# Kernel tuning notes

Hardware: AMD Instinct MI355X
Metric: run time of the kernel (lower is better)

## Reference

```python
import jax, jax.numpy as jnp
import numpy as np

NC = 100000   # output rows of the sparse matrix
NT = 100000   # input columns of the sparse matrix
NNZ = 640000  # number of nonzeros (COO entries)
D = 128       # dense feature width


def setup_inputs() -> dict:
    key = jax.random.key(0)
    k1, k2, k3 = jax.random.split(key, 3)
    mat = jax.random.normal(k1, (NT, D), dtype=jnp.float32)
    row = jax.random.randint(k2, (NNZ,), 0, NC, dtype=jnp.int32)
    col = jax.random.randint(k3, (NNZ,), 0, NT, dtype=jnp.int32)
    return {"mat": mat, "row": row, "col": col}


def reference(mat, row, col):
    # Sparse binary (Nc x Nt) @ dense (Nt x D):
    # out[r] += mat[c] for each nonzero (r, c).
    # The TF original batches gather + tensor_scatter_nd_add over the
    # index list; a single gather + segment_sum computes the same result.
    vals = jnp.take(mat, col, axis=0)                      # [nnz, D]
    out = jax.ops.segment_sum(vals, row, num_segments=NC)  # [Nc, D]
    return out
```

## Files before the change

### kernel.cpp

```cpp
#include <hip/hip_runtime.h>


#define NC_CONST 100000
#define NNZ_CONST 640000
#define D_CONST 128
#define OVF_MAX 65536
#define NXCD 8
#define RANGE 12500
#define PLACE_BLOCKS 2048
#define SCAN_BLK 256
#define NBLK ((NC_CONST + SCAN_BLK - 1) / SCAN_BLK)

typedef float v4f __attribute__((ext_vector_type(4)));
typedef unsigned short u16;
typedef u16 v4u16 __attribute__((ext_vector_type(4)));

template <int CAP>
__global__ __launch_bounds__(256) void place_xcd_kernel(
    const int* __restrict__ row, const int* __restrict__ col,
    int* __restrict__ cnt, int* __restrict__ ovf_cnt,
    int* __restrict__ ovf, int* __restrict__ bucket) {
    const int xcd = blockIdx.x % NXCD;
    const int gidx = blockIdx.x / NXCD;
    const int lo = xcd * RANGE;
    const int hi = lo + RANGE;
    const int nthreads = (PLACE_BLOCKS / NXCD) * 256;
    const int4* row4 = reinterpret_cast<const int4*>(row);
    const int4* col4 = reinterpret_cast<const int4*>(col);
    const int n4 = NNZ_CONST / 4;

    for (int i = gidx * 256 + threadIdx.x; i < n4; i += nthreads) {
        int4 r4 = row4[i];
        int4 c4 = col4[i];
        #pragma unroll
        for (int k = 0; k < 4; ++k) {
            int r = (&r4.x)[k];
            if (r >= lo && r < hi) {
                int c = (&c4.x)[k];
                int idx = atomicAdd(&cnt[r], 1);
                if (idx < CAP) {
                    bucket[(size_t)r * CAP + idx] = c;
                } else {
                    int o = atomicAdd(ovf_cnt, 1);
                    if (o < OVF_MAX) { ovf[2 * o] = r; ovf[2 * o + 1] = c; }
                }
            }
        }
    }
}

__global__ __launch_bounds__(256) void convert_bf16_kernel(
    const float* __restrict__ mat, u16* __restrict__ matb) {
    const long long total4 = (long long)NC_CONST * D_CONST / 4;
    long long i = (long long)blockIdx.x * blockDim.x + threadIdx.x;
    if (i >= total4) return;
    const float4 v = reinterpret_cast<const float4*>(mat)[i];
    v4u16 o;
    #pragma unroll
    for (int k = 0; k < 4; ++k) {
        unsigned u = __float_as_uint((&v.x)[k]);
        o[k] = (u16)((u + 0x7FFFu + ((u >> 16) & 1u)) >> 16);
    }
    reinterpret_cast<v4u16*>(matb)[i] = o;
}

template <int CAP>
__global__ __launch_bounds__(256) void segsum_bf16_kernel(
    const u16* __restrict__ matb, const int* __restrict__ cnt,
    const int* __restrict__ ovf_cnt, const int* __restrict__ ovf,
    const int* __restrict__ bucket, float* __restrict__ out) {
    const int xcd = blockIdx.x % NXCD;
    const int local = blockIdx.x / NXCD;
    int g = xcd * RANGE + local * 8 + (threadIdx.x >> 5);
    int lane = threadIdx.x & 31;
    if (g >= xcd * RANGE + RANGE) return;

    int n = cnt[g];
    if (n > CAP) n = CAP;

    int myc = (lane < n) ? bucket[(size_t)g * CAP + lane] : 0;

    float ax = 0.f, ay = 0.f, az = 0.f, aw = 0.f;
    for (int j = 0; j < n; ++j) {
        int c = __shfl(myc, j, 32);
        const v4u16 b = reinterpret_cast<const v4u16*>(
            matb + (size_t)c * D_CONST)[lane];
        ax += __uint_as_float((unsigned)b[0] << 16);
        ay += __uint_as_float((unsigned)b[1] << 16);
        az += __uint_as_float((unsigned)b[2] << 16);
        aw += __uint_as_float((unsigned)b[3] << 16);
    }

    int novf = *ovf_cnt;
    if (novf > OVF_MAX) novf = OVF_MAX;
    for (int o = 0; o < novf; ++o) {
        if (ovf[2 * o] == g) {
            int c = ovf[2 * o + 1];
            const v4u16 b = reinterpret_cast<const v4u16*>(
                matb + (size_t)c * D_CONST)[lane];
            ax += __uint_as_float((unsigned)b[0] << 16);
            ay += __uint_as_float((unsigned)b[1] << 16);
            az += __uint_as_float((unsigned)b[2] << 16);
            aw += __uint_as_float((unsigned)b[3] << 16);
        }
    }

    v4f r;
    r.x = ax; r.y = ay; r.z = az; r.w = aw;
    __builtin_nontemporal_store(
        r, reinterpret_cast<v4f*>(out + (size_t)g * D_CONST) + lane);
}

template <int CAP>
__global__ __launch_bounds__(256) void segsum_xcd_kernel(
    const float* __restrict__ mat, const int* __restrict__ cnt,
    const int* __restrict__ ovf_cnt, const int* __restrict__ ovf,
    const int* __restrict__ bucket, float* __restrict__ out) {
    const int xcd = blockIdx.x % NXCD;
    const int local = blockIdx.x / NXCD;
    int g = xcd * RANGE + local * 8 + (threadIdx.x >> 5);
    int lane = threadIdx.x & 31;
    if (g >= xcd * RANGE + RANGE) return;

    int n = cnt[g];
    if (n > CAP) n = CAP;
    int myc = (lane < n) ? bucket[(size_t)g * CAP + lane] : 0;

    float ax = 0.f, ay = 0.f, az = 0.f, aw = 0.f;
    for (int j = 0; j < n; ++j) {
        int c = __shfl(myc, j, 32);
        const float4 v =
            reinterpret_cast<const float4*>(mat + (size_t)c * D_CONST)[lane];
        ax += v.x; ay += v.y; az += v.z; aw += v.w;
    }
    int novf = *ovf_cnt;
    if (novf > OVF_MAX) novf = OVF_MAX;
    for (int o = 0; o < novf; ++o) {
        if (ovf[2 * o] == g) {
            int c = ovf[2 * o + 1];
            const float4 v =
                reinterpret_cast<const float4*>(mat + (size_t)c * D_CONST)[lane];
            ax += v.x; ay += v.y; az += v.z; aw += v.w;
        }
    }
    v4f r;
    r.x = ax; r.y = ay; r.z = az; r.w = aw;
    __builtin_nontemporal_store(
        r, reinterpret_cast<v4f*>(out + (size_t)g * D_CONST) + lane);
}

__global__ __launch_bounds__(256) void scatter_add_kernel(
    const float* __restrict__ mat, const int* __restrict__ row,
    const int* __restrict__ col, float* __restrict__ out) {
    int gid = blockIdx.x * blockDim.x + threadIdx.x;
    int nz = gid >> 5;
    int lane = gid & 31;
    if (nz >= NNZ_CONST) return;
    int r = row[nz];
    int c = col[nz];
    const float4 v =
        reinterpret_cast<const float4*>(mat + (size_t)c * D_CONST)[lane];
    float* o = out + (size_t)r * D_CONST + (size_t)lane * 4;
    atomicAdd(o + 0, v.x);
    atomicAdd(o + 1, v.y);
    atomicAdd(o + 2, v.z);
    atomicAdd(o + 3, v.w);
}

extern "C" void kernel_launch(void* const* d_in, const int* in_sizes, int n_in,
                              void* d_out, int out_size, void* d_ws, size_t ws_size,
                              hipStream_t stream) {
    const float* mat = (const float*)d_in[0];
    const int* row   = (const int*)d_in[1];
    const int* col   = (const int*)d_in[2];
    float* out = (float*)d_out;

    constexpr int CAP = 32;
    const size_t ints_common =
        (size_t)NC_CONST + 1 + 2 * OVF_MAX + (size_t)NC_CONST * CAP;
    const size_t need_bf16 =
        (size_t)NC_CONST * D_CONST * sizeof(u16) + ints_common * sizeof(int);
    const size_t need_fp32 = ints_common * sizeof(int);

    const int seg_blocks = ((RANGE + 7) / 8) * NXCD;

    if (ws_size >= need_bf16) {
        u16* matb    = (u16*)d_ws;
        int* cnt     = (int*)(matb + (size_t)NC_CONST * D_CONST);
        int* ovf_cnt = cnt + NC_CONST;
        int* ovf     = ovf_cnt + 1;
        int* bucket  = ovf + 2 * OVF_MAX;

        (void)hipMemsetAsync(cnt, 0, (size_t)(NC_CONST + 1) * sizeof(int), stream);

        place_xcd_kernel<CAP><<<PLACE_BLOCKS, 256, 0, stream>>>(
            row, col, cnt, ovf_cnt, ovf, bucket);

        const long long total4 = (long long)NC_CONST * D_CONST / 4;
        convert_bf16_kernel<<<(int)((total4 + 255) / 256), 256, 0, stream>>>(
            mat, matb);

        segsum_bf16_kernel<CAP><<<seg_blocks, 256, 0, stream>>>(
            matb, cnt, ovf_cnt, ovf, bucket, out);
    } else if (ws_size >= need_fp32) {
        int* cnt     = (int*)d_ws;
        int* ovf_cnt = cnt + NC_CONST;
        int* ovf     = ovf_cnt + 1;
        int* bucket  = ovf + 2 * OVF_MAX;

        (void)hipMemsetAsync(cnt, 0, (size_t)(NC_CONST + 1) * sizeof(int), stream);

        place_xcd_kernel<CAP><<<PLACE_BLOCKS, 256, 0, stream>>>(
            row, col, cnt, ovf_cnt, ovf, bucket);
        segsum_xcd_kernel<CAP><<<seg_blocks, 256, 0, stream>>>(
            mat, cnt, ovf_cnt, ovf, bucket, out);
    } else {
        (void)hipMemsetAsync(out, 0, (size_t)out_size * sizeof(float), stream);
        const long long total = (long long)NNZ_CONST * 32;
        scatter_add_kernel<<<(int)((total + 255) / 256), 256, 0, stream>>>(
            mat, row, col, out);
    }
}
```

Baseline: 175.7 us.

## Fuse bucket placement with bf16 conversion and unroll gather loop by four

Merges the COO bucket-placement kernel and the fp32-to-bf16 conversion into one grid-stride kernel, removing a launch and letting the atomic-bound placement overlap with the streaming conversion. The segment-sum gather loop is unrolled by four so several independent row loads are in flight per warp. Nontemporal loads are added for the mat read and the bucket indices, and the overflow scan is skipped when empty. The fused kernel's fixed grid of 2048 blocks may give the conversion less parallelism than its previous dedicated launch.

```diff
diff --git a/kernel.cpp b/kernel.cpp
--- a/kernel.cpp
+++ b/kernel.cpp
@@ -8,18 +8,22 @@
 #define NXCD 8
 #define RANGE 12500
 #define PLACE_BLOCKS 2048
-#define SCAN_BLK 256
-#define NBLK ((NC_CONST + SCAN_BLK - 1) / SCAN_BLK)
 
 typedef float v4f __attribute__((ext_vector_type(4)));
 typedef unsigned short u16;
 typedef u16 v4u16 __attribute__((ext_vector_type(4)));
 
-template <int CAP>
-__global__ __launch_bounds__(256) void place_xcd_kernel(
+__device__ __forceinline__ float bf16_to_f32(u16 b) {
+    return __uint_as_float((unsigned)b << 16);
+}
+
+template <int CAP>
+__global__ __launch_bounds__(256) void place_convert_kernel(
     const int* __restrict__ row, const int* __restrict__ col,
+    const float* __restrict__ mat,
     int* __restrict__ cnt, int* __restrict__ ovf_cnt,
-    int* __restrict__ ovf, int* __restrict__ bucket) {
+    int* __restrict__ ovf, int* __restrict__ bucket,
+    u16* __restrict__ matb) {
     const int xcd = blockIdx.x % NXCD;
     const int gidx = blockIdx.x / NXCD;
     const int lo = xcd * RANGE;
@@ -47,21 +51,21 @@
             }
         }
     }
-}
-
-__global__ __launch_bounds__(256) void convert_bf16_kernel(
-    const float* __restrict__ mat, u16* __restrict__ matb) {
+
     const long long total4 = (long long)NC_CONST * D_CONST / 4;
-    long long i = (long long)blockIdx.x * blockDim.x + threadIdx.x;
-    if (i >= total4) return;
-    const float4 v = reinterpret_cast<const float4*>(mat)[i];
-    v4u16 o;
-    #pragma unroll
-    for (int k = 0; k < 4; ++k) {
-        unsigned u = __float_as_uint((&v.x)[k]);
-        o[k] = (u16)((u + 0x7FFFu + ((u >> 16) & 1u)) >> 16);
-    }
-    reinterpret_cast<v4u16*>(matb)[i] = o;
+    const long long stride = (long long)gridDim.x * 256;
+    for (long long i = (long long)blockIdx.x * 256 + threadIdx.x;
+         i < total4; i += stride) {
+        const v4f v = __builtin_nontemporal_load(
+            reinterpret_cast<const v4f*>(mat) + i);
+        v4u16 o;
+        #pragma unroll
+        for (int k = 0; k < 4; ++k) {
+            unsigned u = __float_as_uint(v[k]);
+            o[k] = (u16)((u + 0x7FFFu + ((u >> 16) & 1u)) >> 16);
+        }
+        reinterpret_cast<v4u16*>(matb)[i] = o;
+    }
 }
 
 template <int CAP>
@@ -78,30 +82,46 @@
     int n = cnt[g];
     if (n > CAP) n = CAP;
 
-    int myc = (lane < n) ? bucket[(size_t)g * CAP + lane] : 0;
+    int myc = (lane < n)
+        ? __builtin_nontemporal_load(bucket + (size_t)g * CAP + lane) : 0;
 
     float ax = 0.f, ay = 0.f, az = 0.f, aw = 0.f;
-    for (int j = 0; j < n; ++j) {
+    int j = 0;
+    for (; j + 4 <= n; j += 4) {
+        int c0 = __shfl(myc, j + 0, 32);
+        int c1 = __shfl(myc, j + 1, 32);
+        int c2 = __shfl(myc, j + 2, 32);
+        int c3 = __shfl(myc, j + 3, 32);
+        const v4u16 b0 = reinterpret_cast<const v4u16*>(matb + (size_t)c0 * D_CONST)[lane];
+        const v4u16 b1 = reinterpret_cast<const v4u16*>(matb + (size_t)c1 * D_CONST)[lane];
+        const v4u16 b2 = reinterpret_cast<const v4u16*>(matb + (size_t)c2 * D_CONST)[lane];
+        const v4u16 b3 = reinterpret_cast<const v4u16*>(matb + (size_t)c3 * D_CONST)[lane];
+        ax += bf16_to_f32(b0[0]) + bf16_to_f32(b1[0]) + bf16_to_f32(b2[0]) + bf16_to_f32(b3[0]);
+        ay += bf16_to_f32(b0[1]) + bf16_to_f32(b1[1]) + bf16_to_f32(b2[1]) + bf16_to_f32(b3[1]);
+        az += bf16_to_f32(b0[2]) + bf16_to_f32(b1[2]) + bf16_to_f32(b2[2]) + bf16_to_f32(b3[2]);
+        aw += bf16_to_f32(b0[3]) + bf16_to_f32(b1[3]) + bf16_to_f32(b2[3]) + bf16_to_f32(b3[3]);
+    }
+    for (; j < n; ++j) {
         int c = __shfl(myc, j, 32);
-        const v4u16 b = reinterpret_cast<const v4u16*>(
-            matb + (size_t)c * D_CONST)[lane];
-        ax += __uint_as_float((unsigned)b[0] << 16);
-        ay += __uint_as_float((unsigned)b[1] << 16);
-        az += __uint_as_float((unsigned)b[2] << 16);
-        aw += __uint_as_float((unsigned)b[3] << 16);
+        const v4u16 b = reinterpret_cast<const v4u16*>(matb + (size_t)c * D_CONST)[lane];
+        ax += bf16_to_f32(b[0]);
+        ay += bf16_to_f32(b[1]);
+        az += bf16_to_f32(b[2]);
+        aw += bf16_to_f32(b[3]);
     }
 
     int novf = *ovf_cnt;
-    if (novf > OVF_MAX) novf = OVF_MAX;
-    for (int o = 0; o < novf; ++o) {
-        if (ovf[2 * o] == g) {
-            int c = ovf[2 * o + 1];
-            const v4u16 b = reinterpret_cast<const v4u16*>(
-                matb + (size_t)c * D_CONST)[lane];
-            ax += __uint_as_float((unsigned)b[0] << 16);
-            ay += __uint_as_float((unsigned)b[1] << 16);
-            az += __uint_as_float((unsigned)b[2] << 16);
-            aw += __uint_as_float((unsigned)b[3] << 16);
+    if (novf > 0) {
+        if (novf > OVF_MAX) novf = OVF_MAX;
+        for (int o = 0; o < novf; ++o) {
+            if (ovf[2 * o] == g) {
+                int c = ovf[2 * o + 1];
+                const v4u16 b = reinterpret_cast<const v4u16*>(matb + (size_t)c * D_CONST)[lane];
+                ax += bf16_to_f32(b[0]);
+                ay += bf16_to_f32(b[1]);
+                az += bf16_to_f32(b[2]);
+                aw += bf16_to_f32(b[3]);
+            }
         }
     }
 
@@ -147,6 +167,40 @@
     r.x = ax; r.y = ay; r.z = az; r.w = aw;
     __builtin_nontemporal_store(
         r, reinterpret_cast<v4f*>(out + (size_t)g * D_CONST) + lane);
+}
+
+template <int CAP>
+__global__ __launch_bounds__(256) void place_xcd_kernel(
+    const int* __restrict__ row, const int* __restrict__ col,
+    int* __restrict__ cnt, int* __restrict__ ovf_cnt,
+    int* __restrict__ ovf, int* __restrict__ bucket) {
+    const int xcd = blockIdx.x % NXCD;
+    const int gidx = blockIdx.x / NXCD;
+    const int lo = xcd * RANGE;
+    const int hi = lo + RANGE;
+    const int nthreads = (PLACE_BLOCKS / NXCD) * 256;
+    const int4* row4 = reinterpret_cast<const int4*>(row);
+    const int4* col4 = reinterpret_cast<const int4*>(col);
+    const int n4 = NNZ_CONST / 4;
+
+    for (int i = gidx * 256 + threadIdx.x; i < n4; i += nthreads) {
+        int4 r4 = row4[i];
+        int4 c4 = col4[i];
+        #pragma unroll
+        for (int k = 0; k < 4; ++k) {
+            int r = (&r4.x)[k];
+            if (r >= lo && r < hi) {
+                int c = (&c4.x)[k];
+                int idx = atomicAdd(&cnt[r], 1);
+                if (idx < CAP) {
+                    bucket[(size_t)r * CAP + idx] = c;
+                } else {
+                    int o = atomicAdd(ovf_cnt, 1);
+                    if (o < OVF_MAX) { ovf[2 * o] = r; ovf[2 * o + 1] = c; }
+                }
+            }
+        }
+    }
 }
 
 __global__ __launch_bounds__(256) void scatter_add_kernel(
@@ -193,12 +247,8 @@
 
         (void)hipMemsetAsync(cnt, 0, (size_t)(NC_CONST + 1) * sizeof(int), stream);
 
-        place_xcd_kernel<CAP><<<PLACE_BLOCKS, 256, 0, stream>>>(
-            row, col, cnt, ovf_cnt, ovf, bucket);
-
-        const long long total4 = (long long)NC_CONST * D_CONST / 4;
-        convert_bf16_kernel<<<(int)((total4 + 255) / 256), 256, 0, stream>>>(
-            mat, matb);
+        place_convert_kernel<CAP><<<PLACE_BLOCKS, 256, 0, stream>>>(
+            row, col, mat, cnt, ovf_cnt, ovf, bucket, matb);
 
         segsum_bf16_kernel<CAP><<<seg_blocks, 256, 0, stream>>>(
             matb, cnt, ovf_cnt, ovf, bucket, out);
```

Measured after the change: 162.8 us. 7.4% less time.
